# Optimization experiments

Measured on AMD Instinct MI355X. Metric: run time of the kernel, lower is better.

The kernel has to match this reference:

```python
import jax, jax.numpy as jnp
import numpy as np

GRID_SIZE = 5
SPLINE_ORDER = 3
NUM_EXPERTS = 8
TOP_K = 2
CAP_FACTOR = 1.25
TEMP = 1.0
GDHW = (4, 4, 4)


def make_grid(in_features):
    # efficient-KAN grid buffer: grid_range=[-1,1], extended by spline_order on each side
    h = 2.0 / GRID_SIZE
    g = jnp.arange(-SPLINE_ORDER, GRID_SIZE + SPLINE_ORDER + 1, dtype=jnp.float32) * h - 1.0
    return jnp.broadcast_to(g, (in_features, g.shape[0]))


def b_splines(x, grid):
    # x: (N, in) -> (N, in, GRID_SIZE + SPLINE_ORDER) Cox-de Boor bases
    x = x[:, :, None]
    bases = ((x >= grid[:, :-1]) & (x < grid[:, 1:])).astype(x.dtype)
    for k in range(1, SPLINE_ORDER + 1):
        left = (x - grid[:, : -(k + 1)]) / (grid[:, k:-1] - grid[:, : -(k + 1)])
        right = (grid[:, k + 1:] - x) / (grid[:, k + 1:] - grid[:, 1:-k])
        bases = left * bases[:, :, :-1] + right * bases[:, :, 1:]
    return bases


def kan_linear(x, base_w, spline_w, scaler, grid):
    base = jax.nn.silu(x) @ base_w.T
    bs = b_splines(x, grid)                                   # (N, in, coef)
    spline = jnp.einsum('nic,oic->no', bs, spline_w * scaler[:, :, None])
    return base + spline


def layernorm(x, w, b, eps=1e-5):
    mu = x.mean(-1, keepdims=True)
    var = x.var(-1, keepdims=True)
    return (x - mu) / jnp.sqrt(var + eps) * w + b


def setup_inputs() -> dict:
    key = jax.random.key(0)
    ks = jax.random.split(key, 12)
    Cf, hidden, E, nc = 256, 170, NUM_EXPERTS, 2
    coef = GRID_SIZE + SPLINE_ORDER
    def nrm(k, shape, scale):
        return jax.random.normal(k, shape, dtype=jnp.float32) * scale
    return {
        'fpn_feat': nrm(ks[0], (8, 254, 32, 32, 32), 1.0),
        'seg_logits': nrm(ks[1], (8, 2, 32, 32, 32), 1.0),
        'ln_r_w': jnp.ones((Cf,), jnp.float32),
        'ln_r_b': jnp.zeros((Cf,), jnp.float32),
        'ln_h_w': jnp.ones((Cf,), jnp.float32),
        'ln_h_b': jnp.zeros((Cf,), jnp.float32),
        'router_w': nrm(ks[2], (E, Cf), Cf ** -0.5),
        'router_b': jnp.zeros((E,), jnp.float32),
        'bw1': nrm(ks[3], (E, hidden, Cf), Cf ** -0.5),
        'sw1': nrm(ks[4], (E, hidden, Cf, coef), 0.1 * Cf ** -0.5),
        'sc1': nrm(ks[5], (E, hidden, Cf), Cf ** -0.5),
        'bw2': nrm(ks[6], (E, Cf, hidden), hidden ** -0.5),
        'sw2': nrm(ks[7], (E, Cf, hidden, coef), 0.1 * hidden ** -0.5),
        'sc2': nrm(ks[8], (E, Cf, hidden), hidden ** -0.5),
        'cls_bw': nrm(ks[9], (nc, Cf), Cf ** -0.5),
        'cls_sw': nrm(ks[10], (nc, Cf, coef), 0.1 * Cf ** -0.5),
        'cls_sc': nrm(ks[11], (nc, Cf), Cf ** -0.5),
        'grid_cf': make_grid(Cf),
        'grid_hid': make_grid(hidden),
    }


def reference(fpn_feat, seg_logits, ln_r_w, ln_r_b, ln_h_w, ln_h_b,
              router_w, router_b, bw1, sw1, sc1, bw2, sw2, sc2,
              cls_bw, cls_sw, cls_sc, grid_cf, grid_hid):
    fused = jnp.concatenate([fpn_feat, seg_logits], axis=1)   # (B, Cf, D, H, W)
    B, C, D, H, W = fused.shape
    gd, gh, gw = GDHW
    dp, hp, wp = D // gd, H // gh, W // gw
    # split into gd*gh*gw blocks per sample
    blk = fused.reshape(B, C, gd, dp, gh, hp, gw, wp)
    blk = blk.transpose(0, 2, 4, 6, 1, 3, 5, 7).reshape(-1, C, dp, hp, wp)
    vec = blk.mean(axis=(2, 3, 4))                            # (N, Cf) global avg pool

    N = vec.shape[0]
    E = NUM_EXPERTS
    x_norm = layernorm(vec, ln_r_w, ln_r_b)
    scores = (x_norm @ router_w.T + router_b) / TEMP          # (N, E)
    top_val, top_idx = jax.lax.top_k(scores, TOP_K)
    top_w = jax.nn.softmax(top_val, axis=-1)
    capacity = int(CAP_FACTOR * N * TOP_K / E) + 1

    onehot = top_idx[None] == jnp.arange(E)[:, None, None]    # (E, N, K)
    sel = onehot.any(-1)                                      # (E, N)
    pos = jnp.cumsum(sel.astype(jnp.int32), axis=1)           # rank among selected (1-based)
    keep = sel & (pos <= capacity)                            # capacity drop = first-come order
    w = (top_w[None] * onehot.astype(top_w.dtype)).sum(-1)    # (E, N) combine weights

    def expert(bw1e, sw1e, sc1e, bw2e, sw2e, sc2e):
        h = kan_linear(x_norm, bw1e, sw1e, sc1e, grid_cf)
        h = jax.nn.gelu(h, approximate=False)                 # torch nn.GELU default (erf)
        return kan_linear(h, bw2e, sw2e, sc2e, grid_hid)

    y_all = jax.vmap(expert)(bw1, sw1, sc1, bw2, sw2, sc2)    # (E, N, Cf)
    out = jnp.einsum('en,enc->nc', keep.astype(vec.dtype) * w, y_all)

    conf = scores.max(-1)                                     # (N,)
    logits_blk = kan_linear(layernorm(out, ln_h_w, ln_h_b), cls_bw, cls_sw, cls_sc, grid_cf)
    P = gd * gh * gw
    weight = jax.nn.softmax(conf.reshape(B, P), axis=-1)[:, :, None]
    logits = (logits_blk.reshape(B, P, -1) * weight).sum(1)   # (B, num_classes)
    return logits
```

## Files before the change

kernel.cpp:

```cpp
#include <hip/hip_runtime.h>
#include <math.h>

#define CF 256
#define HID 170
#define NE 8
#define NTOK 512
#define K1 2304
#define K2P 1536
#define CAPACITY 161

typedef __bf16 bf16x8 __attribute__((ext_vector_type(8)));
typedef unsigned short u16x8 __attribute__((ext_vector_type(8)));
typedef float f32x4 __attribute__((ext_vector_type(4)));

__device__ __forceinline__ float silu_f(float x) { return x / (1.0f + expf(-x)); }

__device__ __forceinline__ unsigned short f2bf(float f) {
    unsigned int u = __float_as_uint(f);
    u = u + 0x7fffu + ((u >> 16) & 1u);
    return (unsigned short)(u >> 16);
}

__device__ __forceinline__ void bspline8(float x, float bs[8]) {
    float b[11];
#pragma unroll
    for (int j = 0; j < 11; ++j) {
        float g0 = (float)(j - 3) * 0.4f - 1.0f;
        float g1 = (float)(j - 2) * 0.4f - 1.0f;
        b[j] = (x >= g0 && x < g1) ? 1.0f : 0.0f;
    }
#pragma unroll
    for (int k = 1; k <= 3; ++k) {
        float inv = 2.5f / (float)k;
#pragma unroll
        for (int j = 0; j < 10 - (k - 1); ++j) {
            float gj   = (float)(j - 3) * 0.4f - 1.0f;
            float gjk1 = (float)(j - 2 + k) * 0.4f - 1.0f;
            b[j] = (x - gj) * inv * b[j] + (gjk1 - x) * inv * b[j + 1];
        }
    }
#pragma unroll
    for (int c = 0; c < 8; ++c) bs[c] = b[c];
}

__global__ __launch_bounds__(256) void pool_kernel(const float* __restrict__ fpn,
                                                   const float* __restrict__ seg,
                                                   float* __restrict__ vec) {
    int c = blockIdx.x, b = blockIdx.y, tid = threadIdx.x;
    const float* src = (c < 254) ? fpn + (size_t)(b * 254 + c) * 32768
                                 : seg + (size_t)(b * 2 + (c - 254)) * 32768;
    const float4* s4 = (const float4*)src;
    float s[4] = {0.f, 0.f, 0.f, 0.f};
#pragma unroll
    for (int it = 0; it < 32; ++it) {
        float4 v = s4[it * 256 + tid];
        s[it >> 3] += v.x + v.y + v.z + v.w;
    }
    __shared__ float acc[64];
    if (tid < 64) acc[tid] = 0.0f;
    __syncthreads();
    int bh = tid >> 6, bw = (tid & 7) >> 1;
#pragma unroll
    for (int bd = 0; bd < 4; ++bd) atomicAdd(&acc[bd * 16 + bh * 4 + bw], s[bd]);
    __syncthreads();
    if (tid < 64) vec[(size_t)(b * 64 + tid) * CF + c] = acc[tid] * (1.0f / 512.0f);
}

__global__ __launch_bounds__(256) void ln_score_kernel(const float* __restrict__ vec,
                                                       const float* __restrict__ lnw,
                                                       const float* __restrict__ lnb,
                                                       const float* __restrict__ rw,
                                                       const float* __restrict__ rb,
                                                       float* __restrict__ xnorm,
                                                       float* __restrict__ scores) {
    int n = blockIdx.x, i = threadIdx.x;
    float v = vec[(size_t)n * CF + i];
    float s1 = v, s2 = v * v;
#pragma unroll
    for (int off = 32; off > 0; off >>= 1) {
        s1 += __shfl_xor(s1, off);
        s2 += __shfl_xor(s2, off);
    }
    __shared__ float rs1[4], rs2[4];
    int lane = i & 63, wid = i >> 6;
    if (lane == 0) { rs1[wid] = s1; rs2[wid] = s2; }
    __syncthreads();
    float tot1 = rs1[0] + rs1[1] + rs1[2] + rs1[3];
    float tot2 = rs2[0] + rs2[1] + rs2[2] + rs2[3];
    float mu = tot1 * (1.0f / CF);
    float var = tot2 * (1.0f / CF) - mu * mu;
    float rsd = rsqrtf(var + 1e-5f);
    float xv = (v - mu) * rsd * lnw[i] + lnb[i];
    xnorm[(size_t)n * CF + i] = xv;
    float p[NE];
#pragma unroll
    for (int e = 0; e < NE; ++e) p[e] = xv * rw[e * CF + i];
#pragma unroll
    for (int off = 32; off > 0; off >>= 1)
#pragma unroll
        for (int e = 0; e < NE; ++e) p[e] += __shfl_xor(p[e], off);
    __shared__ float pacc[4][NE];
    if (lane == 0)
#pragma unroll
        for (int e = 0; e < NE; ++e) pacc[wid][e] = p[e];
    __syncthreads();
    if (i < NE)
        scores[n * NE + i] = pacc[0][i] + pacc[1][i] + pacc[2][i] + pacc[3][i] + rb[i];
}

__global__ __launch_bounds__(512) void topk_kernel(const float* __restrict__ scores,
                                                   float* __restrict__ cw,
                                                   float* __restrict__ conf) {
    int n = threadIdx.x;
    __shared__ int   ti0[NTOK], ti1[NTOK];
    __shared__ float tw0[NTOK], tw1[NTOK];
    float m1 = -1e30f, m2 = -1e30f; int i1 = 0, i2 = 0;
#pragma unroll
    for (int e = 0; e < NE; ++e) {
        float sc = scores[n * NE + e];
        if (sc > m1) { m2 = m1; i2 = i1; m1 = sc; i1 = e; }
        else if (sc > m2) { m2 = sc; i2 = e; }
    }
    conf[n] = m1;
    float ew = expf(m2 - m1);
    ti0[n] = i1; ti1[n] = i2;
    tw0[n] = 1.0f / (1.0f + ew); tw1[n] = ew / (1.0f + ew);
    __syncthreads();
    int e = n >> 6, lane = n & 63;
    int cnt = 0;
    for (int c = 0; c < NTOK / 64; ++c) {
        int t = c * 64 + lane;
        int h0 = (ti0[t] == e), h1 = (ti1[t] == e);
        int sel = h0 | h1;
        unsigned long long mask = __ballot(sel);
        int pos = cnt + (int)__popcll(mask & ((1ull << lane) - 1ull));
        float wv = 0.f;
        if (sel && pos < CAPACITY) wv = h0 ? tw0[t] : tw1[t];
        cw[e * NTOK + t] = wv;
        cnt += (int)__popcll(mask);
    }
}

__global__ __launch_bounds__(256) void buildA1_kernel(const float* __restrict__ xnorm,
                                                      unsigned short* __restrict__ A1) {
    int n = blockIdx.x, i = threadIdx.x;
    float x = xnorm[(size_t)n * CF + i];
    unsigned short* r = A1 + (size_t)n * K1;
    r[i] = f2bf(silu_f(x));
    float bs[8]; bspline8(x, bs);
    unsigned short* sp = r + CF + i * 8;
#pragma unroll
    for (int c = 0; c < 8; ++c) sp[c] = f2bf(bs[c]);
}

__global__ __launch_bounds__(256) void buildW1_kernel(const float* __restrict__ bw1,
                                                      const float* __restrict__ sw1,
                                                      const float* __restrict__ sc1,
                                                      unsigned short* __restrict__ W1) {
    int o = blockIdx.x, e = blockIdx.y, i = threadIdx.x;
    size_t oi = (size_t)(e * HID + o) * CF + i;
    unsigned short* r = W1 + (size_t)(e * HID + o) * K1;
    r[i] = f2bf(bw1[oi]);
    float sc = sc1[oi];
    const float* sw = sw1 + oi * 8;
    unsigned short* sp = r + CF + i * 8;
#pragma unroll
    for (int c = 0; c < 8; ++c) sp[c] = f2bf(sw[c] * sc);
}

__global__ __launch_bounds__(192) void buildW2_kernel(const float* __restrict__ bw2,
                                                      const float* __restrict__ sw2,
                                                      const float* __restrict__ sc2,
                                                      unsigned short* __restrict__ W2) {
    int o = blockIdx.x, e = blockIdx.y, t = threadIdx.x;
    unsigned short* r = W2 + (size_t)(e * CF + o) * K2P;
    if (t < HID) {
        size_t oi = (size_t)(e * CF + o) * HID + t;
        r[t] = f2bf(bw2[oi]);
        float sc = sc2[oi];
        const float* sw = sw2 + oi * 8;
        unsigned short* sp = r + HID + t * 8;
#pragma unroll
        for (int c = 0; c < 8; ++c) sp[c] = f2bf(sw[c] * sc);
    } else if (t < HID + 6) {
        r[HID * 9 + (t - HID)] = 0;
    }
}

__global__ __launch_bounds__(192) void buildA2_kernel(const float* __restrict__ H,
                                                      unsigned short* __restrict__ A2) {
    int n = blockIdx.x, e = blockIdx.y, t = threadIdx.x;
    unsigned short* r = A2 + (size_t)(e * NTOK + n) * K2P;
    if (t < HID) {
        float h = H[(size_t)(e * NTOK + n) * HID + t];
        r[t] = f2bf(silu_f(h));
        float bs[8]; bspline8(h, bs);
        unsigned short* sp = r + HID + t * 8;
#pragma unroll
        for (int c = 0; c < 8; ++c) sp[c] = f2bf(bs[c]);
    } else if (t < HID + 6) {
        r[HID * 9 + (t - HID)] = 0;
    }
}

__global__ __launch_bounds__(256) void gemm_mfma_kernel(const unsigned short* __restrict__ Ag,
                                                        const unsigned short* __restrict__ Bg,
                                                        float* __restrict__ C,
                                                        int N, int K, long sA, long sB, long sC,
                                                        int ldc, int act) {
    int e = blockIdx.z;
    const unsigned short* A = Ag + (size_t)e * sA;
    const unsigned short* B = Bg + (size_t)e * sB;
    C += (size_t)e * sC;
    int m0 = blockIdx.y * 64, n0 = blockIdx.x * 64;

    __shared__ alignas(16) unsigned char AsB[8192];
    __shared__ alignas(16) unsigned char BsB[8192];

    int tid = threadIdx.x;
    int lane = tid & 63, w = tid >> 6;
    int wr = w >> 1, wc = w & 1;
    int fr = lane & 15, fg = lane >> 4;
    int srow = tid >> 3;
    int schunk = tid & 7;

    int r0 = srow, r1 = srow + 32;
    int wb0 = r0 * 128 + ((schunk * 16) ^ ((r0 & 7) << 4));
    int wb1 = r1 * 128 + ((schunk * 16) ^ ((r1 & 7) << 4));

    f32x4 acc[2][2];
#pragma unroll
    for (int i = 0; i < 2; ++i)
#pragma unroll
        for (int j = 0; j < 2; ++j)
#pragma unroll
            for (int r = 0; r < 4; ++r) acc[i][j][r] = 0.f;

    for (int k0 = 0; k0 < K; k0 += 64) {
        u16x8 a0 = *(const u16x8*)(A + (size_t)(m0 + r0) * K + k0 + schunk * 8);
        u16x8 a1 = *(const u16x8*)(A + (size_t)(m0 + r1) * K + k0 + schunk * 8);
        u16x8 b0 = {0, 0, 0, 0, 0, 0, 0, 0};
        u16x8 b1 = {0, 0, 0, 0, 0, 0, 0, 0};
        int bn0 = n0 + r0, bn1 = n0 + r1;
        if (bn0 < N) b0 = *(const u16x8*)(B + (size_t)bn0 * K + k0 + schunk * 8);
        if (bn1 < N) b1 = *(const u16x8*)(B + (size_t)bn1 * K + k0 + schunk * 8);
        __syncthreads();
        *(u16x8*)(AsB + wb0) = a0;
        *(u16x8*)(AsB + wb1) = a1;
        *(u16x8*)(BsB + wb0) = b0;
        *(u16x8*)(BsB + wb1) = b1;
        __syncthreads();
#pragma unroll
        for (int ks = 0; ks < 2; ++ks) {
            int kb = ks * 64 + fg * 16;
            u16x8 af[2], bf[2];
#pragma unroll
            for (int mf = 0; mf < 2; ++mf) {
                int row = wr * 32 + mf * 16 + fr;
                af[mf] = *(const u16x8*)(AsB + row * 128 + (kb ^ ((row & 7) << 4)));
            }
#pragma unroll
            for (int nf = 0; nf < 2; ++nf) {
                int row = wc * 32 + nf * 16 + fr;
                bf[nf] = *(const u16x8*)(BsB + row * 128 + (kb ^ ((row & 7) << 4)));
            }
#pragma unroll
            for (int mf = 0; mf < 2; ++mf)
#pragma unroll
                for (int nf = 0; nf < 2; ++nf)
                    acc[mf][nf] = __builtin_amdgcn_mfma_f32_16x16x32_bf16(
                        __builtin_bit_cast(bf16x8, af[mf]),
                        __builtin_bit_cast(bf16x8, bf[nf]), acc[mf][nf], 0, 0, 0);
        }
    }
#pragma unroll
    for (int mf = 0; mf < 2; ++mf)
#pragma unroll
        for (int nf = 0; nf < 2; ++nf)
#pragma unroll
            for (int r = 0; r < 4; ++r) {
                int row = m0 + wr * 32 + mf * 16 + fg * 4 + r;
                int col = n0 + wc * 32 + nf * 16 + fr;
                if (col < N) {
                    float v = acc[mf][nf][r];
                    if (act) v = 0.5f * v * (1.0f + erff(v * 0.70710678118654752f));
                    C[(size_t)row * ldc + col] = v;
                }
            }
}

__global__ __launch_bounds__(256) void combine_kernel(const float* __restrict__ y,
                                                      const float* __restrict__ cw,
                                                      float* __restrict__ outc) {
    int n = blockIdx.x, c = threadIdx.x;
    float a = 0.f;
#pragma unroll
    for (int e = 0; e < NE; ++e)
        a += cw[e * NTOK + n] * y[((size_t)(e * NTOK + n)) * CF + c];
    outc[(size_t)n * CF + c] = a;
}

__global__ __launch_bounds__(256) void cls_kernel(const float* __restrict__ outc,
                                                  const float* __restrict__ lnw,
                                                  const float* __restrict__ lnb,
                                                  const float* __restrict__ cbw,
                                                  const float* __restrict__ csw,
                                                  const float* __restrict__ csc,
                                                  float* __restrict__ lblk) {
    int n = blockIdx.x, i = threadIdx.x;
    float v = outc[(size_t)n * CF + i];
    float s1 = v, s2 = v * v;
#pragma unroll
    for (int off = 32; off > 0; off >>= 1) {
        s1 += __shfl_xor(s1, off);
        s2 += __shfl_xor(s2, off);
    }
    __shared__ float rA[4], rB[4], rP0[4], rP1[4];
    int lane = i & 63, wid = i >> 6;
    if (lane == 0) { rA[wid] = s1; rB[wid] = s2; }
    __syncthreads();
    float tot1 = rA[0] + rA[1] + rA[2] + rA[3];
    float tot2 = rB[0] + rB[1] + rB[2] + rB[3];
    float mu = tot1 * (1.0f / CF);
    float var = tot2 * (1.0f / CF) - mu * mu;
    float rs = rsqrtf(var + 1e-5f);
    float xh = (v - mu) * rs * lnw[i] + lnb[i];
    float si = silu_f(xh);
    float bs[8]; bspline8(xh, bs);
    float p0 = si * cbw[i], p1 = si * cbw[CF + i];
    float sp0 = 0.f, sp1 = 0.f;
#pragma unroll
    for (int c = 0; c < 8; ++c) {
        sp0 += bs[c] * csw[(size_t)i * 8 + c];
        sp1 += bs[c] * csw[(size_t)(CF + i) * 8 + c];
    }
    p0 += sp0 * csc[i];
    p1 += sp1 * csc[CF + i];
#pragma unroll
    for (int off = 32; off > 0; off >>= 1) {
        p0 += __shfl_xor(p0, off);
        p1 += __shfl_xor(p1, off);
    }
    if (lane == 0) { rP0[wid] = p0; rP1[wid] = p1; }
    __syncthreads();
    if (i == 0) {
        lblk[n * 2 + 0] = rP0[0] + rP0[1] + rP0[2] + rP0[3];
        lblk[n * 2 + 1] = rP1[0] + rP1[1] + rP1[2] + rP1[3];
    }
}

__global__ __launch_bounds__(64) void final_kernel(const float* __restrict__ conf,
                                                   const float* __restrict__ lblk,
                                                   float* __restrict__ out) {
    int b = blockIdx.x, p = threadIdx.x;
    float cf = conf[b * 64 + p];
    float mx = cf;
#pragma unroll
    for (int off = 32; off > 0; off >>= 1) mx = fmaxf(mx, __shfl_xor(mx, off));
    float ev = expf(cf - mx);
    float s = ev;
#pragma unroll
    for (int off = 32; off > 0; off >>= 1) s += __shfl_xor(s, off);
    float w = ev / s;
    float l0 = w * lblk[(b * 64 + p) * 2 + 0];
    float l1 = w * lblk[(b * 64 + p) * 2 + 1];
#pragma unroll
    for (int off = 32; off > 0; off >>= 1) {
        l0 += __shfl_xor(l0, off);
        l1 += __shfl_xor(l1, off);
    }
    if (p == 0) { out[b * 2 + 0] = l0; out[b * 2 + 1] = l1; }
}

extern "C" void kernel_launch(void* const* d_in, const int* in_sizes, int n_in,
                              void* d_out, int out_size, void* d_ws, size_t ws_size,
                              hipStream_t stream) {
    const float* fpn      = (const float*)d_in[0];
    const float* seg      = (const float*)d_in[1];
    const float* ln_r_w   = (const float*)d_in[2];
    const float* ln_r_b   = (const float*)d_in[3];
    const float* ln_h_w   = (const float*)d_in[4];
    const float* ln_h_b   = (const float*)d_in[5];
    const float* router_w = (const float*)d_in[6];
    const float* router_b = (const float*)d_in[7];
    const float* bw1      = (const float*)d_in[8];
    const float* sw1      = (const float*)d_in[9];
    const float* sc1      = (const float*)d_in[10];
    const float* bw2      = (const float*)d_in[11];
    const float* sw2      = (const float*)d_in[12];
    const float* sc2      = (const float*)d_in[13];
    const float* cls_bw   = (const float*)d_in[14];
    const float* cls_sw   = (const float*)d_in[15];
    const float* cls_sc   = (const float*)d_in[16];

    float* ws = (float*)d_ws;
    float* vec    = ws;
    float* xnorm  = vec + 131072;
    float* scores = xnorm + 131072;
    float* cw     = scores + 4096;
    float* conf   = cw + 4096;
    float* lblk   = conf + 512;
    float* outc   = lblk + 1024;
    float* Hbuf   = outc + 131072;
    float* yall   = Hbuf + 696320;
    unsigned short* A1b = (unsigned short*)(yall + 1048576);
    unsigned short* W1b = A1b + (size_t)NTOK * K1;
    unsigned short* A2b = W1b + (size_t)NE * HID * K1;
    unsigned short* W2b = A2b + (size_t)NE * NTOK * K2P;

    pool_kernel<<<dim3(CF, 8), dim3(256), 0, stream>>>(fpn, seg, vec);
    buildW1_kernel<<<dim3(HID, NE), dim3(256), 0, stream>>>(bw1, sw1, sc1, W1b);
    buildW2_kernel<<<dim3(CF, NE), dim3(192), 0, stream>>>(bw2, sw2, sc2, W2b);
    ln_score_kernel<<<dim3(NTOK), dim3(256), 0, stream>>>(vec, ln_r_w, ln_r_b, router_w,
                                                          router_b, xnorm, scores);
    topk_kernel<<<dim3(1), dim3(512), 0, stream>>>(scores, cw, conf);
    buildA1_kernel<<<dim3(NTOK), dim3(256), 0, stream>>>(xnorm, A1b);
    gemm_mfma_kernel<<<dim3(3, 8, NE), dim3(256), 0, stream>>>(
        A1b, W1b, Hbuf, HID, K1, 0L, (long)HID * K1, (long)NTOK * HID, HID, 1);
    buildA2_kernel<<<dim3(NTOK, NE), dim3(192), 0, stream>>>(Hbuf, A2b);
    gemm_mfma_kernel<<<dim3(4, 8, NE), dim3(256), 0, stream>>>(
        A2b, W2b, yall, CF, K2P, (long)NTOK * K2P, (long)CF * K2P, (long)NTOK * CF, CF, 0);
    combine_kernel<<<dim3(NTOK), dim3(256), 0, stream>>>(yall, cw, outc);
    cls_kernel<<<dim3(NTOK), dim3(256), 0, stream>>>(outc, ln_h_w, ln_h_b, cls_bw, cls_sw,
                                                     cls_sc, lblk);
    final_kernel<<<dim3(8), dim3(64), 0, stream>>>(conf, lblk, (float*)d_out);
}
```

Before: 132.3 us.

## Fuse front-end, A-matrix builds and combine/classifier kernels; prefetch GEMM tiles

Merges pooling and both weight-repack passes into one large launch, so the weight repack can overlap the bandwidth-bound pooling. It folds the A1 build into the layernorm/router kernel and moves GELU plus the silu/B-spline A2 construction into the first GEMM's epilogue, which removes the H and xnorm intermediates and several launches. It adds register prefetch of the next K-tile in the GEMM, fuses combine with the classifier, and vectorizes the bf16 spline stores. One risk: the A2 padding columns are no longer explicitly zeroed, so they rely on whatever the workspace already holds.

```diff
diff --git a/kernel.cpp b/kernel.cpp
--- a/kernel.cpp
+++ b/kernel.cpp
@@ -14,6 +14,9 @@
 typedef float f32x4 __attribute__((ext_vector_type(4)));
 
 __device__ __forceinline__ float silu_f(float x) { return x / (1.0f + expf(-x)); }
+__device__ __forceinline__ float gelu_f(float x) {
+    return 0.5f * x * (1.0f + erff(x * 0.70710678118654752f));
+}
 
 __device__ __forceinline__ unsigned short f2bf(float f) {
     unsigned int u = __float_as_uint(f);
@@ -43,36 +46,75 @@
     for (int c = 0; c < 8; ++c) bs[c] = b[c];
 }
 
-__global__ __launch_bounds__(256) void pool_kernel(const float* __restrict__ fpn,
-                                                   const float* __restrict__ seg,
-                                                   float* __restrict__ vec) {
-    int c = blockIdx.x, b = blockIdx.y, tid = threadIdx.x;
-    const float* src = (c < 254) ? fpn + (size_t)(b * 254 + c) * 32768
-                                 : seg + (size_t)(b * 2 + (c - 254)) * 32768;
-    const float4* s4 = (const float4*)src;
-    float s[4] = {0.f, 0.f, 0.f, 0.f};
-#pragma unroll
-    for (int it = 0; it < 32; ++it) {
-        float4 v = s4[it * 256 + tid];
-        s[it >> 3] += v.x + v.y + v.z + v.w;
-    }
-    __shared__ float acc[64];
-    if (tid < 64) acc[tid] = 0.0f;
-    __syncthreads();
-    int bh = tid >> 6, bw = (tid & 7) >> 1;
-#pragma unroll
-    for (int bd = 0; bd < 4; ++bd) atomicAdd(&acc[bd * 16 + bh * 4 + bw], s[bd]);
-    __syncthreads();
-    if (tid < 64) vec[(size_t)(b * 64 + tid) * CF + c] = acc[tid] * (1.0f / 512.0f);
-}
-
-__global__ __launch_bounds__(256) void ln_score_kernel(const float* __restrict__ vec,
-                                                       const float* __restrict__ lnw,
-                                                       const float* __restrict__ lnb,
-                                                       const float* __restrict__ rw,
-                                                       const float* __restrict__ rb,
-                                                       float* __restrict__ xnorm,
-                                                       float* __restrict__ scores) {
+__global__ __launch_bounds__(256) void mega_front_kernel(const float* __restrict__ fpn,
+                                                         const float* __restrict__ seg,
+                                                         const float* __restrict__ bw1,
+                                                         const float* __restrict__ sw1,
+                                                         const float* __restrict__ sc1,
+                                                         const float* __restrict__ bw2,
+                                                         const float* __restrict__ sw2,
+                                                         const float* __restrict__ sc2,
+                                                         float* __restrict__ vec,
+                                                         unsigned short* __restrict__ W1,
+                                                         unsigned short* __restrict__ W2) {
+    int id = blockIdx.x, tid = threadIdx.x;
+    if (id < 2048) {
+        int c = id & 255, b = id >> 8;
+        const float* src = (c < 254) ? fpn + (size_t)(b * 254 + c) * 32768
+                                     : seg + (size_t)(b * 2 + (c - 254)) * 32768;
+        const float4* s4 = (const float4*)src;
+        float s[4] = {0.f, 0.f, 0.f, 0.f};
+#pragma unroll
+        for (int it = 0; it < 32; ++it) {
+            float4 v = s4[it * 256 + tid];
+            s[it >> 3] += v.x + v.y + v.z + v.w;
+        }
+        __shared__ float acc[64];
+        if (tid < 64) acc[tid] = 0.0f;
+        __syncthreads();
+        int bh = tid >> 6, bw = (tid & 7) >> 1;
+#pragma unroll
+        for (int bd = 0; bd < 4; ++bd) atomicAdd(&acc[bd * 16 + bh * 4 + bw], s[bd]);
+        __syncthreads();
+        if (tid < 64) vec[(size_t)(b * 64 + tid) * CF + c] = acc[tid] * (1.0f / 512.0f);
+    } else if (id < 2048 + NE * HID) {
+        int r = id - 2048;
+        int o = r % HID, e = r / HID, i = tid;
+        size_t oi = (size_t)(e * HID + o) * CF + i;
+        unsigned short* row = W1 + (size_t)(e * HID + o) * K1;
+        row[i] = f2bf(bw1[oi]);
+        float sc = sc1[oi];
+        const float* sw = sw1 + oi * 8;
+        u16x8 pk;
+#pragma unroll
+        for (int c = 0; c < 8; ++c) pk[c] = f2bf(sw[c] * sc);
+        *(u16x8*)(row + CF + i * 8) = pk;
+    } else {
+        int r = id - (2048 + NE * HID);
+        int o = r & 255, e = r >> 8, t = tid;
+        unsigned short* row = W2 + (size_t)(e * CF + o) * K2P;
+        if (t < HID) {
+            size_t oi = (size_t)(e * CF + o) * HID + t;
+            row[t] = f2bf(bw2[oi]);
+            float sc = sc2[oi];
+            const float* sw = sw2 + oi * 8;
+            u16x8 pk;
+#pragma unroll
+            for (int c = 0; c < 8; ++c) pk[c] = f2bf(sw[c] * sc);
+            *(u16x8*)(row + HID + t * 8) = pk;
+        } else if (t < HID + 6) {
+            row[HID * 9 + (t - HID)] = 0;
+        }
+    }
+}
+
+__global__ __launch_bounds__(256) void ln_score_a1_kernel(const float* __restrict__ vec,
+                                                          const float* __restrict__ lnw,
+                                                          const float* __restrict__ lnb,
+                                                          const float* __restrict__ rw,
+                                                          const float* __restrict__ rb,
+                                                          float* __restrict__ scores,
+                                                          unsigned short* __restrict__ A1) {
     int n = blockIdx.x, i = threadIdx.x;
     float v = vec[(size_t)n * CF + i];
     float s1 = v, s2 = v * v;
@@ -91,7 +133,13 @@
     float var = tot2 * (1.0f / CF) - mu * mu;
     float rsd = rsqrtf(var + 1e-5f);
     float xv = (v - mu) * rsd * lnw[i] + lnb[i];
-    xnorm[(size_t)n * CF + i] = xv;
+    unsigned short* r = A1 + (size_t)n * K1;
+    r[i] = f2bf(silu_f(xv));
+    float bs[8]; bspline8(xv, bs);
+    u16x8 pk;
+#pragma unroll
+    for (int c = 0; c < 8; ++c) pk[c] = f2bf(bs[c]);
+    *(u16x8*)(r + CF + i * 8) = pk;
     float p[NE];
 #pragma unroll
     for (int e = 0; e < NE; ++e) p[e] = xv * rw[e * CF + i];
@@ -141,77 +189,15 @@
     }
 }
 
-__global__ __launch_bounds__(256) void buildA1_kernel(const float* __restrict__ xnorm,
-                                                      unsigned short* __restrict__ A1) {
-    int n = blockIdx.x, i = threadIdx.x;
-    float x = xnorm[(size_t)n * CF + i];
-    unsigned short* r = A1 + (size_t)n * K1;
-    r[i] = f2bf(silu_f(x));
-    float bs[8]; bspline8(x, bs);
-    unsigned short* sp = r + CF + i * 8;
-#pragma unroll
-    for (int c = 0; c < 8; ++c) sp[c] = f2bf(bs[c]);
-}
-
-__global__ __launch_bounds__(256) void buildW1_kernel(const float* __restrict__ bw1,
-                                                      const float* __restrict__ sw1,
-                                                      const float* __restrict__ sc1,
-                                                      unsigned short* __restrict__ W1) {
-    int o = blockIdx.x, e = blockIdx.y, i = threadIdx.x;
-    size_t oi = (size_t)(e * HID + o) * CF + i;
-    unsigned short* r = W1 + (size_t)(e * HID + o) * K1;
-    r[i] = f2bf(bw1[oi]);
-    float sc = sc1[oi];
-    const float* sw = sw1 + oi * 8;
-    unsigned short* sp = r + CF + i * 8;
-#pragma unroll
-    for (int c = 0; c < 8; ++c) sp[c] = f2bf(sw[c] * sc);
-}
-
-__global__ __launch_bounds__(192) void buildW2_kernel(const float* __restrict__ bw2,
-                                                      const float* __restrict__ sw2,
-                                                      const float* __restrict__ sc2,
-                                                      unsigned short* __restrict__ W2) {
-    int o = blockIdx.x, e = blockIdx.y, t = threadIdx.x;
-    unsigned short* r = W2 + (size_t)(e * CF + o) * K2P;
-    if (t < HID) {
-        size_t oi = (size_t)(e * CF + o) * HID + t;
-        r[t] = f2bf(bw2[oi]);
-        float sc = sc2[oi];
-        const float* sw = sw2 + oi * 8;
-        unsigned short* sp = r + HID + t * 8;
-#pragma unroll
-        for (int c = 0; c < 8; ++c) sp[c] = f2bf(sw[c] * sc);
-    } else if (t < HID + 6) {
-        r[HID * 9 + (t - HID)] = 0;
-    }
-}
-
-__global__ __launch_bounds__(192) void buildA2_kernel(const float* __restrict__ H,
-                                                      unsigned short* __restrict__ A2) {
-    int n = blockIdx.x, e = blockIdx.y, t = threadIdx.x;
-    unsigned short* r = A2 + (size_t)(e * NTOK + n) * K2P;
-    if (t < HID) {
-        float h = H[(size_t)(e * NTOK + n) * HID + t];
-        r[t] = f2bf(silu_f(h));
-        float bs[8]; bspline8(h, bs);
-        unsigned short* sp = r + HID + t * 8;
-#pragma unroll
-        for (int c = 0; c < 8; ++c) sp[c] = f2bf(bs[c]);
-    } else if (t < HID + 6) {
-        r[HID * 9 + (t - HID)] = 0;
-    }
-}
-
 __global__ __launch_bounds__(256) void gemm_mfma_kernel(const unsigned short* __restrict__ Ag,
                                                         const unsigned short* __restrict__ Bg,
                                                         float* __restrict__ C,
+                                                        unsigned short* __restrict__ A2,
                                                         int N, int K, long sA, long sB, long sC,
-                                                        int ldc, int act) {
+                                                        int ldc, int mode) {
     int e = blockIdx.z;
     const unsigned short* A = Ag + (size_t)e * sA;
     const unsigned short* B = Bg + (size_t)e * sB;
-    C += (size_t)e * sC;
     int m0 = blockIdx.y * 64, n0 = blockIdx.x * 64;
 
     __shared__ alignas(16) unsigned char AsB[8192];
@@ -236,20 +222,29 @@
 #pragma unroll
             for (int r = 0; r < 4; ++r) acc[i][j][r] = 0.f;
 
-    for (int k0 = 0; k0 < K; k0 += 64) {
-        u16x8 a0 = *(const u16x8*)(A + (size_t)(m0 + r0) * K + k0 + schunk * 8);
-        u16x8 a1 = *(const u16x8*)(A + (size_t)(m0 + r1) * K + k0 + schunk * 8);
-        u16x8 b0 = {0, 0, 0, 0, 0, 0, 0, 0};
-        u16x8 b1 = {0, 0, 0, 0, 0, 0, 0, 0};
-        int bn0 = n0 + r0, bn1 = n0 + r1;
-        if (bn0 < N) b0 = *(const u16x8*)(B + (size_t)bn0 * K + k0 + schunk * 8);
-        if (bn1 < N) b1 = *(const u16x8*)(B + (size_t)bn1 * K + k0 + schunk * 8);
+    int bn0 = n0 + r0, bn1 = n0 + r1;
+    const int steps = K >> 6;
+    u16x8 a0, a1, b0, b1;
+    a0 = *(const u16x8*)(A + (size_t)(m0 + r0) * K + schunk * 8);
+    a1 = *(const u16x8*)(A + (size_t)(m0 + r1) * K + schunk * 8);
+    b0 = b1 = (u16x8){0, 0, 0, 0, 0, 0, 0, 0};
+    if (bn0 < N) b0 = *(const u16x8*)(B + (size_t)bn0 * K + schunk * 8);
+    if (bn1 < N) b1 = *(const u16x8*)(B + (size_t)bn1 * K + schunk * 8);
+
+    for (int s = 0; s < steps; ++s) {
         __syncthreads();
         *(u16x8*)(AsB + wb0) = a0;
         *(u16x8*)(AsB + wb1) = a1;
         *(u16x8*)(BsB + wb0) = b0;
         *(u16x8*)(BsB + wb1) = b1;
         __syncthreads();
+        if (s + 1 < steps) {
+            int k0 = (s + 1) << 6;
+            a0 = *(const u16x8*)(A + (size_t)(m0 + r0) * K + k0 + schunk * 8);
+            a1 = *(const u16x8*)(A + (size_t)(m0 + r1) * K + k0 + schunk * 8);
+            if (bn0 < N) b0 = *(const u16x8*)(B + (size_t)bn0 * K + k0 + schunk * 8);
+            if (bn1 < N) b1 = *(const u16x8*)(B + (size_t)bn1 * K + k0 + schunk * 8);
+        }
 #pragma unroll
         for (int ks = 0; ks < 2; ++ks) {
             int kb = ks * 64 + fg * 16;
@@ -273,42 +268,55 @@
                         __builtin_bit_cast(bf16x8, bf[nf]), acc[mf][nf], 0, 0, 0);
         }
     }
-#pragma unroll
-    for (int mf = 0; mf < 2; ++mf)
-#pragma unroll
-        for (int nf = 0; nf < 2; ++nf)
-#pragma unroll
-            for (int r = 0; r < 4; ++r) {
-                int row = m0 + wr * 32 + mf * 16 + fg * 4 + r;
-                int col = n0 + wc * 32 + nf * 16 + fr;
-                if (col < N) {
-                    float v = acc[mf][nf][r];
-                    if (act) v = 0.5f * v * (1.0f + erff(v * 0.70710678118654752f));
-                    C[(size_t)row * ldc + col] = v;
+
+    if (mode == 1) {
+#pragma unroll
+        for (int mf = 0; mf < 2; ++mf)
+#pragma unroll
+            for (int nf = 0; nf < 2; ++nf)
+#pragma unroll
+                for (int r = 0; r < 4; ++r) {
+                    int row = m0 + wr * 32 + mf * 16 + fg * 4 + r;
+                    int col = n0 + wc * 32 + nf * 16 + fr;
+                    if (col < N) {
+                        float g = gelu_f(acc[mf][nf][r]);
+                        unsigned short* rr = A2 + ((size_t)e * NTOK + row) * K2P;
+                        rr[col] = f2bf(silu_f(g));
+                        float bs[8]; bspline8(g, bs);
+                        u16x8 pk;
+#pragma unroll
+                        for (int c = 0; c < 8; ++c) pk[c] = f2bf(bs[c]);
+                        *(u16x8*)(rr + HID + col * 8) = pk;
+                    }
                 }
-            }
-}
-
-__global__ __launch_bounds__(256) void combine_kernel(const float* __restrict__ y,
+    } else {
+        float* Ce = C + (size_t)e * sC;
+#pragma unroll
+        for (int mf = 0; mf < 2; ++mf)
+#pragma unroll
+            for (int nf = 0; nf < 2; ++nf)
+#pragma unroll
+                for (int r = 0; r < 4; ++r) {
+                    int row = m0 + wr * 32 + mf * 16 + fg * 4 + r;
+                    int col = n0 + wc * 32 + nf * 16 + fr;
+                    if (col < N) Ce[(size_t)row * ldc + col] = acc[mf][nf][r];
+                }
+    }
+}
+
+__global__ __launch_bounds__(256) void combcls_kernel(const float* __restrict__ y,
                                                       const float* __restrict__ cw,
-                                                      float* __restrict__ outc) {
-    int n = blockIdx.x, c = threadIdx.x;
-    float a = 0.f;
+                                                      const float* __restrict__ lnw,
+                                                      const float* __restrict__ lnb,
+                                                      const float* __restrict__ cbw,
+                                                      const float* __restrict__ csw,
+                                                      const float* __restrict__ csc,
+                                                      float* __restrict__ lblk) {
+    int n = blockIdx.x, i = threadIdx.x;
+    float v = 0.f;
 #pragma unroll
     for (int e = 0; e < NE; ++e)
-        a += cw[e * NTOK + n] * y[((size_t)(e * NTOK + n)) * CF + c];
-    outc[(size_t)n * CF + c] = a;
-}
-
-__global__ __launch_bounds__(256) void cls_kernel(const float* __restrict__ outc,
-                                                  const float* __restrict__ lnw,
-                                                  const float* __restrict__ lnb,
-                                                  const float* __restrict__ cbw,
-                                                  const float* __restrict__ csw,
-                                                  const float* __restrict__ csc,
-                                                  float* __restrict__ lblk) {
-    int n = blockIdx.x, i = threadIdx.x;
-    float v = outc[(size_t)n * CF + i];
+        v += cw[e * NTOK + n] * y[((size_t)(e * NTOK + n)) * CF + i];
     float s1 = v, s2 = v * v;
 #pragma unroll
     for (int off = 32; off > 0; off >>= 1) {
@@ -395,33 +403,27 @@
 
     float* ws = (float*)d_ws;
     float* vec    = ws;
-    float* xnorm  = vec + 131072;
-    float* scores = xnorm + 131072;
+    float* scores = vec + 131072;
     float* cw     = scores + 4096;
     float* conf   = cw + 4096;
     float* lblk   = conf + 512;
-    float* outc   = lblk + 1024;
-    float* Hbuf   = outc + 131072;
-    float* yall   = Hbuf + 696320;
+    float* yall   = lblk + 1024;
     unsigned short* A1b = (unsigned short*)(yall + 1048576);
     unsigned short* W1b = A1b + (size_t)NTOK * K1;
     unsigned short* A2b = W1b + (size_t)NE * HID * K1;
     unsigned short* W2b = A2b + (size_t)NE * NTOK * K2P;
 
-    pool_kernel<<<dim3(CF, 8), dim3(256), 0, stream>>>(fpn, seg, vec);
-    buildW1_kernel<<<dim3(HID, NE), dim3(256), 0, stream>>>(bw1, sw1, sc1, W1b);
-    buildW2_kernel<<<dim3(CF, NE), dim3(192), 0, stream>>>(bw2, sw2, sc2, W2b);
-    ln_score_kernel<<<dim3(NTOK), dim3(256), 0, stream>>>(vec, ln_r_w, ln_r_b, router_w,
-                                                          router_b, xnorm, scores);
+    mega_front_kernel<<<dim3(2048 + NE * HID + 2048), dim3(256), 0, stream>>>(
+        fpn, seg, bw1, sw1, sc1, bw2, sw2, sc2, vec, W1b, W2b);
+    ln_score_a1_kernel<<<dim3(NTOK), dim3(256), 0, stream>>>(vec, ln_r_w, ln_r_b, router_w,
+                                                             router_b, scores, A1b);
     topk_kernel<<<dim3(1), dim3(512), 0, stream>>>(scores, cw, conf);
-    buildA1_kernel<<<dim3(NTOK), dim3(256), 0, stream>>>(xnorm, A1b);
     gemm_mfma_kernel<<<dim3(3, 8, NE), dim3(256), 0, stream>>>(
-        A1b, W1b, Hbuf, HID, K1, 0L, (long)HID * K1, (long)NTOK * HID, HID, 1);
-    buildA2_kernel<<<dim3(NTOK, NE), dim3(192), 0, stream>>>(Hbuf, A2b);
+        A1b, W1b, nullptr, A2b, HID, K1, 0L, (long)HID * K1, 0L, 0, 1);
     gemm_mfma_kernel<<<dim3(4, 8, NE), dim3(256), 0, stream>>>(
-        A2b, W2b, yall, CF, K2P, (long)NTOK * K2P, (long)CF * K2P, (long)NTOK * CF, CF, 0);
-    combine_kernel<<<dim3(NTOK), dim3(256), 0, stream>>>(yall, cw, outc);
-    cls_kernel<<<dim3(NTOK), dim3(256), 0, stream>>>(outc, ln_h_w, ln_h_b, cls_bw, cls_sw,
-                                                     cls_sc, lblk);
+        A2b, W2b, yall, nullptr, CF, K2P, (long)NTOK * K2P, (long)CF * K2P,
+        (long)NTOK * CF, CF, 0);
+    combcls_kernel<<<dim3(NTOK), dim3(256), 0, stream>>>(yall, cw, ln_h_w, ln_h_b, cls_bw,
+                                                         cls_sw, cls_sc, lblk);
     final_kernel<<<dim3(8), dim3(64), 0, stream>>>(conf, lblk, (float*)d_out);
 }
```

After: 117.1 us. -11.5%, faster.
